# Performance work log

Measured on AMD Instinct MI355X. Metric: run time of the kernel, lower is better.

## Reference

```python
import jax, jax.numpy as jnp
import numpy as np

B, S, D = 2, 2048, 1024
H = 16
HD = D // H  # 64


def setup_inputs() -> dict:
    key = jax.random.key(0)
    ks = jax.random.split(key, 6)
    scale = 0.02
    return {
        "x": jax.random.normal(ks[0], (B, S, D), dtype=jnp.float32),
        "Wq": jax.random.normal(ks[1], (D, D), dtype=jnp.float32) * scale,
        "Wk": jax.random.normal(ks[2], (D, D), dtype=jnp.float32) * scale,
        "Wv": jax.random.normal(ks[3], (D, D), dtype=jnp.float32) * scale,
        "Wo": jax.random.normal(ks[4], (D, D), dtype=jnp.float32) * scale,
        "bo": jnp.zeros((D,), dtype=jnp.float32),
    }


def reference(x, Wq, Wk, Wv, Wo, bo):
    b, n, _ = x.shape
    # QKV projections (weights stored as [d_in, d_out]; no qkv bias)
    q = (x @ Wq).reshape(b, n, H, HD).transpose(0, 2, 1, 3)  # [b,h,n,hd]
    k = (x @ Wk).reshape(b, n, H, HD).transpose(0, 2, 1, 3)
    v = (x @ Wv).reshape(b, n, H, HD).transpose(0, 2, 1, 3)
    # raw scores, causal mask (upper-triangular -> -inf), THEN scale (as in source)
    scores = jnp.einsum("bhqd,bhkd->bhqk", q, k)
    causal = jnp.triu(jnp.ones((n, n), dtype=bool), k=1)
    scores = jnp.where(causal, -jnp.inf, scores)
    attn = jax.nn.softmax(scores / np.sqrt(HD).astype(np.float32), axis=-1)
    # dropout p=0.0 -> identity
    ctx = jnp.einsum("bhqk,bhkd->bqhd", attn, v).reshape(b, n, H * HD)
    return ctx @ Wo + bo
```

## Files before the change

kernel.cpp:

```cpp
#include <hip/hip_runtime.h>
#include <math.h>

#define BB 2
#define SS 2048
#define DD 1024
#define HH 16
#define HDIM 64
#define NTOK (BB * SS)

typedef __attribute__((ext_vector_type(8))) short short8;
typedef __attribute__((ext_vector_type(4))) short short4v;
typedef __attribute__((ext_vector_type(4))) float f32x4;

__device__ __forceinline__ short f2bf(float f) {
    unsigned u = __builtin_bit_cast(unsigned, f);
    u = (u + 0x7FFFu + ((u >> 16) & 1u)) >> 16;
    return (short)u;
}

__device__ __forceinline__ void gl_lds16(const short* g, short* l) {
    __builtin_amdgcn_global_load_lds(
        (const __attribute__((address_space(1))) void*)g,
        (__attribute__((address_space(3))) void*)l, 16, 0, 0);
}

__global__ __launch_bounds__(256) void convert_x_kernel(
    const float* __restrict__ x, short* __restrict__ xbf)
{
    const size_t idx = ((size_t)blockIdx.x * 256 + threadIdx.x) * 8;
    float4 a = *reinterpret_cast<const float4*>(x + idx);
    float4 b = *reinterpret_cast<const float4*>(x + idx + 4);
    short8 o;
    o[0] = f2bf(a.x); o[1] = f2bf(a.y); o[2] = f2bf(a.z); o[3] = f2bf(a.w);
    o[4] = f2bf(b.x); o[5] = f2bf(b.y); o[6] = f2bf(b.z); o[7] = f2bf(b.w);
    *reinterpret_cast<short8*>(xbf + idx) = o;
}

__global__ __launch_bounds__(256) void convw_kernel(
    const float* __restrict__ Wq, const float* __restrict__ Wk,
    const float* __restrict__ Wv, const float* __restrict__ Wo,
    short* __restrict__ Wtq, short* __restrict__ Wtk,
    short* __restrict__ Wtv, short* __restrict__ Wto)
{
    const int z = blockIdx.z;
    const float* W = (z == 0) ? Wq : (z == 1) ? Wk : (z == 2) ? Wv : Wo;
    short* Wt = (z == 0) ? Wtq : (z == 1) ? Wtk : (z == 2) ? Wtv : Wto;
    const int k0 = blockIdx.x * 64, n0 = blockIdx.y * 64;
    __shared__ float T[64][65];
    const int tid = threadIdx.x;
    for (int i = tid; i < 1024; i += 256) {
        int r = i >> 4, c4 = (i & 15) * 4;
        float4 v = *reinterpret_cast<const float4*>(W + (size_t)(k0 + r) * DD + n0 + c4);
        T[r][c4 + 0] = v.x; T[r][c4 + 1] = v.y; T[r][c4 + 2] = v.z; T[r][c4 + 3] = v.w;
    }
    __syncthreads();
    for (int i = tid; i < 512; i += 256) {
        int n = i >> 3, k8 = (i & 7) * 8;
        short8 o;
        #pragma unroll
        for (int j = 0; j < 8; ++j) o[j] = f2bf(T[k8 + j][n]);
        *reinterpret_cast<short8*>(Wt + (size_t)(n0 + n) * DD + k0 + k8) = o;
    }
}

__global__ __launch_bounds__(256) void qkv_mfma_kernel(
    const short* __restrict__ xbf,
    const short* __restrict__ Wtq, const short* __restrict__ Wtk,
    const short* __restrict__ Wtv,
    short* __restrict__ Q, short* __restrict__ K, short* __restrict__ Vt)
{
    const int which = blockIdx.z;
    const short* Wt = (which == 0) ? Wtq : (which == 1) ? Wtk : Wtv;

    const int row0 = blockIdx.y * 128;
    const int col0 = blockIdx.x * 128;
    __shared__ short As[128 * 32];
    __shared__ short Bs[128 * 32];

    const int tid = threadIdx.x;
    const int w = tid >> 6, lane = tid & 63;
    const int wm = (w >> 1) * 64, wn = (w & 1) * 64;
    const int lrow = lane & 15, lgrp = lane >> 4, lk = lgrp * 8;

    f32x4 acc[4][4];
    #pragma unroll
    for (int m = 0; m < 4; ++m)
        #pragma unroll
        for (int n = 0; n < 4; ++n) acc[m][n] = (f32x4){0.f, 0.f, 0.f, 0.f};

    for (int k0 = 0; k0 < DD; k0 += 32) {
        #pragma unroll
        for (int c = 0; c < 2; ++c) {
            int slot = c * 256 + tid;
            int r = slot >> 2, cb = (slot & 3) * 8;
            gl_lds16(xbf + (size_t)(row0 + r) * DD + k0 + cb, As + slot * 8);
            gl_lds16(Wt + (size_t)(col0 + r) * DD + k0 + cb, Bs + slot * 8);
        }
        __syncthreads();
        short8 af[4], bf_[4];
        #pragma unroll
        for (int m = 0; m < 4; ++m)
            af[m] = *reinterpret_cast<const short8*>(&As[(wm + m * 16 + lrow) * 32 + lk]);
        #pragma unroll
        for (int n = 0; n < 4; ++n)
            bf_[n] = *reinterpret_cast<const short8*>(&Bs[(wn + n * 16 + lrow) * 32 + lk]);
        #pragma unroll
        for (int m = 0; m < 4; ++m)
            #pragma unroll
            for (int n = 0; n < 4; ++n)
                acc[m][n] = __builtin_amdgcn_mfma_f32_16x16x32_bf16(
                    af[m], bf_[n], acc[m][n], 0, 0, 0);
        __syncthreads();
    }

    if (which < 2) {
        short* Out = (which == 0) ? Q : K;
        #pragma unroll
        for (int m = 0; m < 4; ++m) {
            #pragma unroll
            for (int r = 0; r < 4; ++r) {
                int tok = row0 + wm + m * 16 + lgrp * 4 + r;
                int bb = tok >> 11, s = tok & 2047;
                #pragma unroll
                for (int n = 0; n < 4; ++n) {
                    int d = col0 + wn + n * 16 + lrow;
                    int hh = d >> 6, hd = d & 63;
                    Out[(((size_t)bb * HH + hh) * SS + s) * HDIM + hd] = f2bf(acc[m][n][r]);
                }
            }
        }
    } else {
        #pragma unroll
        for (int m = 0; m < 4; ++m) {
            int tok0 = row0 + wm + m * 16 + lgrp * 4;
            int bb = tok0 >> 11, s0 = tok0 & 2047;
            #pragma unroll
            for (int n = 0; n < 4; ++n) {
                int d = col0 + wn + n * 16 + lrow;
                int hh = d >> 6, hd = d & 63;
                short4v pk;
                pk[0] = f2bf(acc[m][n][0]); pk[1] = f2bf(acc[m][n][1]);
                pk[2] = f2bf(acc[m][n][2]); pk[3] = f2bf(acc[m][n][3]);
                *reinterpret_cast<short4v*>(
                    Vt + (((size_t)bb * HH + hh) * HDIM + hd) * SS + s0) = pk;
            }
        }
    }
}

__global__ __launch_bounds__(256) void attn_mfma_kernel(
    const short* __restrict__ Q, const short* __restrict__ K,
    const short* __restrict__ Vt, short* __restrict__ ctx)
{
    const int qt = 63 - (int)blockIdx.x;
    const int h = blockIdx.y, b = blockIdx.z;
    const int q0 = qt * 32;

    __shared__ float merge_buf[4][32][68];
    __shared__ float mbuf[4][32], lbuf[4][32];

    const int tid = threadIdx.x;
    const int w = tid >> 6, lane = tid & 63;
    const int lrow = lane & 15, lgrp = lane >> 4;
    short (*Ps)[72] = reinterpret_cast<short (*)[72]>(&merge_buf[w][0][0]);

    const size_t hb = ((size_t)b * HH + h) * SS;
    const float SC = 0.125f * 1.44269504088896340736f;

    short8 qf[2][2];
    const short* Qb = Q + (hb + q0) * HDIM;
    #pragma unroll
    for (int mf = 0; mf < 2; ++mf)
        #pragma unroll
        for (int kf = 0; kf < 2; ++kf)
            qf[mf][kf] = *reinterpret_cast<const short8*>(
                Qb + (mf * 16 + lrow) * HDIM + kf * 32 + lgrp * 8);

    f32x4 Oa[2][4];
    float mrun[2], lrun[2];
    #pragma unroll
    for (int mf = 0; mf < 2; ++mf) {
        #pragma unroll
        for (int nf = 0; nf < 4; ++nf) Oa[mf][nf] = (f32x4){0.f, 0.f, 0.f, 0.f};
        mrun[mf] = -INFINITY; lrun[mf] = 0.f;
    }

    const int nkb = (qt >> 1) + 1;
    const short* Kbase = K + hb * HDIM;
    const short* Vtb = Vt + ((size_t)b * HH + h) * HDIM * SS;

    for (int kb = w; kb < nkb; kb += 4) {
        const int kv0 = kb * 64;

        short8 kfr[4][2];
        #pragma unroll
        for (int nf = 0; nf < 4; ++nf)
            #pragma unroll
            for (int kf = 0; kf < 2; ++kf)
                kfr[nf][kf] = *reinterpret_cast<const short8*>(
                    Kbase + (size_t)(kv0 + nf * 16 + lrow) * HDIM + kf * 32 + lgrp * 8);

        f32x4 s[4][2];
        #pragma unroll
        for (int nf = 0; nf < 4; ++nf)
            #pragma unroll
            for (int mf = 0; mf < 2; ++mf) s[nf][mf] = (f32x4){0.f, 0.f, 0.f, 0.f};
        #pragma unroll
        for (int nf = 0; nf < 4; ++nf)
            #pragma unroll
            for (int mf = 0; mf < 2; ++mf)
                #pragma unroll
                for (int kf = 0; kf < 2; ++kf)
                    s[nf][mf] = __builtin_amdgcn_mfma_f32_16x16x32_bf16(
                        kfr[nf][kf], qf[mf][kf], s[nf][mf], 0, 0, 0);

        const bool diag = (kv0 + 63 > q0);
        #pragma unroll
        for (int nf = 0; nf < 4; ++nf)
            #pragma unroll
            for (int mf = 0; mf < 2; ++mf)
                #pragma unroll
                for (int r = 0; r < 4; ++r) {
                    float v = s[nf][mf][r] * SC;
                    if (diag) {
                        int qg = q0 + mf * 16 + lrow;
                        int kg = kv0 + nf * 16 + lgrp * 4 + r;
                        if (kg > qg) v = -INFINITY;
                    }
                    s[nf][mf][r] = v;
                }

        float alpha[2];
        #pragma unroll
        for (int mf = 0; mf < 2; ++mf) {
            float pm = -INFINITY;
            #pragma unroll
            for (int nf = 0; nf < 4; ++nf)
                #pragma unroll
                for (int r = 0; r < 4; ++r) pm = fmaxf(pm, s[nf][mf][r]);
            pm = fmaxf(pm, __shfl_xor(pm, 16));
            pm = fmaxf(pm, __shfl_xor(pm, 32));
            float mn = fmaxf(mrun[mf], pm);
            alpha[mf] = exp2f(mrun[mf] - mn);
            mrun[mf] = mn;
            float rs = 0.f;
            #pragma unroll
            for (int nf = 0; nf < 4; ++nf)
                #pragma unroll
                for (int r = 0; r < 4; ++r) {
                    float p = exp2f(s[nf][mf][r] - mn);
                    s[nf][mf][r] = p;
                    rs += p;
                }
            rs += __shfl_xor(rs, 16);
            rs += __shfl_xor(rs, 32);
            lrun[mf] = lrun[mf] * alpha[mf] + rs;
        }

        #pragma unroll
        for (int mf = 0; mf < 2; ++mf)
            #pragma unroll
            for (int nf = 0; nf < 4; ++nf) {
                short4v pk;
                pk[0] = f2bf(s[nf][mf][0]); pk[1] = f2bf(s[nf][mf][1]);
                pk[2] = f2bf(s[nf][mf][2]); pk[3] = f2bf(s[nf][mf][3]);
                *reinterpret_cast<short4v*>(&Ps[mf * 16 + lrow][nf * 16 + lgrp * 4]) = pk;
            }
        asm volatile("s_waitcnt lgkmcnt(0)" ::: "memory");
        __builtin_amdgcn_sched_barrier(0);

        short8 pa[2][2], vb_[4][2];
        #pragma unroll
        for (int mf = 0; mf < 2; ++mf)
            #pragma unroll
            for (int kf = 0; kf < 2; ++kf)
                pa[mf][kf] = *reinterpret_cast<const short8*>(
                    &Ps[mf * 16 + lrow][kf * 32 + lgrp * 8]);

        #pragma unroll
        for (int nf = 0; nf < 4; ++nf)
            #pragma unroll
            for (int kf = 0; kf < 2; ++kf)
                vb_[nf][kf] = *reinterpret_cast<const short8*>(
                    Vtb + (size_t)(nf * 16 + lrow) * SS + kv0 + kf * 32 + lgrp * 8);

        #pragma unroll
        for (int mf = 0; mf < 2; ++mf)
            #pragma unroll
            for (int r = 0; r < 4; ++r) {
                float a = __shfl(alpha[mf], lgrp * 4 + r);
                #pragma unroll
                for (int nf = 0; nf < 4; ++nf) Oa[mf][nf][r] *= a;
            }

        #pragma unroll
        for (int mf = 0; mf < 2; ++mf)
            #pragma unroll
            for (int nf = 0; nf < 4; ++nf)
                #pragma unroll
                for (int kf = 0; kf < 2; ++kf)
                    Oa[mf][nf] = __builtin_amdgcn_mfma_f32_16x16x32_bf16(
                        pa[mf][kf], vb_[nf][kf], Oa[mf][nf], 0, 0, 0);
    }

    #pragma unroll
    for (int mf = 0; mf < 2; ++mf) {
        if (lgrp == 0) {
            mbuf[w][mf * 16 + lrow] = mrun[mf];
            lbuf[w][mf * 16 + lrow] = lrun[mf];
        }
        #pragma unroll
        for (int r = 0; r < 4; ++r) {
            int row = mf * 16 + lgrp * 4 + r;
            #pragma unroll
            for (int nf = 0; nf < 4; ++nf)
                merge_buf[w][row][nf * 16 + lrow] = Oa[mf][nf][r];
        }
    }
    __syncthreads();

    {
        const int row = tid >> 3;
        const int c0 = (tid & 7) * 8;
        float m0 = mbuf[0][row], m1 = mbuf[1][row];
        float m2 = mbuf[2][row], m3 = mbuf[3][row];
        float mg = fmaxf(fmaxf(m0, m1), fmaxf(m2, m3));
        float w0 = exp2f(m0 - mg), w1 = exp2f(m1 - mg);
        float w2 = exp2f(m2 - mg), w3 = exp2f(m3 - mg);
        float lg = w0 * lbuf[0][row] + w1 * lbuf[1][row] +
                   w2 * lbuf[2][row] + w3 * lbuf[3][row];
        float rl = 1.f / lg;
        short8 o8;
        #pragma unroll
        for (int j = 0; j < 8; ++j) {
            float o = w0 * merge_buf[0][row][c0 + j] + w1 * merge_buf[1][row][c0 + j] +
                      w2 * merge_buf[2][row][c0 + j] + w3 * merge_buf[3][row][c0 + j];
            o8[j] = f2bf(o * rl);
        }
        const int tok = b * SS + q0 + row;
        *reinterpret_cast<short8*>(ctx + (size_t)tok * DD + h * HDIM + c0) = o8;
    }
}

__global__ __launch_bounds__(256) void out_mfma_kernel(
    const short* __restrict__ ctxbf, const short* __restrict__ Wto,
    const float* __restrict__ bo, float* __restrict__ out)
{
    const int row0 = blockIdx.y * 128;
    const int col0 = blockIdx.x * 128;
    __shared__ short As[128 * 32];
    __shared__ short Bs[128 * 32];

    const int tid = threadIdx.x;
    const int w = tid >> 6, lane = tid & 63;
    const int wm = (w >> 1) * 64, wn = (w & 1) * 64;
    const int lrow = lane & 15, lgrp = lane >> 4, lk = lgrp * 8;

    f32x4 acc[4][4];
    #pragma unroll
    for (int m = 0; m < 4; ++m)
        #pragma unroll
        for (int n = 0; n < 4; ++n) acc[m][n] = (f32x4){0.f, 0.f, 0.f, 0.f};

    for (int k0 = 0; k0 < DD; k0 += 32) {
        #pragma unroll
        for (int c = 0; c < 2; ++c) {
            int slot = c * 256 + tid;
            int r = slot >> 2, cb = (slot & 3) * 8;
            gl_lds16(ctxbf + (size_t)(row0 + r) * DD + k0 + cb, As + slot * 8);
            gl_lds16(Wto + (size_t)(col0 + r) * DD + k0 + cb, Bs + slot * 8);
        }
        __syncthreads();
        short8 af[4], bf_[4];
        #pragma unroll
        for (int m = 0; m < 4; ++m)
            af[m] = *reinterpret_cast<const short8*>(&As[(wm + m * 16 + lrow) * 32 + lk]);
        #pragma unroll
        for (int n = 0; n < 4; ++n)
            bf_[n] = *reinterpret_cast<const short8*>(&Bs[(wn + n * 16 + lrow) * 32 + lk]);
        #pragma unroll
        for (int m = 0; m < 4; ++m)
            #pragma unroll
            for (int n = 0; n < 4; ++n)
                acc[m][n] = __builtin_amdgcn_mfma_f32_16x16x32_bf16(
                    af[m], bf_[n], acc[m][n], 0, 0, 0);
        __syncthreads();
    }

    #pragma unroll
    for (int m = 0; m < 4; ++m) {
        #pragma unroll
        for (int r = 0; r < 4; ++r) {
            int tok = row0 + wm + m * 16 + lgrp * 4 + r;
            #pragma unroll
            for (int n = 0; n < 4; ++n) {
                int d = col0 + wn + n * 16 + lrow;
                out[(size_t)tok * DD + d] = acc[m][n][r] + bo[d];
            }
        }
    }
}

extern "C" void kernel_launch(void* const* d_in, const int* in_sizes, int n_in,
                              void* d_out, int out_size, void* d_ws, size_t ws_size,
                              hipStream_t stream) {
    const float* x  = (const float*)d_in[0];
    const float* Wq = (const float*)d_in[1];
    const float* Wk = (const float*)d_in[2];
    const float* Wv = (const float*)d_in[3];
    const float* Wo = (const float*)d_in[4];
    const float* bo = (const float*)d_in[5];
    float* out = (float*)d_out;

    const size_t plane = (size_t)NTOK * DD;
    const size_t wsz   = (size_t)DD * DD;
    short* xbf  = (short*)d_ws;
    short* Wtq  = xbf + plane;
    short* Wtk  = Wtq + wsz;
    short* Wtv  = Wtk + wsz;
    short* Wto  = Wtv + wsz;
    short* Qb   = Wto + wsz;
    short* Kb   = Qb + plane;
    short* Vtb  = Kb + plane;
    short* ctxb = Vtb + plane;

    convert_x_kernel<<<dim3((unsigned)(plane / (256 * 8))), 256, 0, stream>>>(x, xbf);
    convw_kernel<<<dim3(16, 16, 4), 256, 0, stream>>>(Wq, Wk, Wv, Wo, Wtq, Wtk, Wtv, Wto);
    qkv_mfma_kernel<<<dim3(DD / 128, NTOK / 128, 3), 256, 0, stream>>>(
        xbf, Wtq, Wtk, Wtv, Qb, Kb, Vtb);
    attn_mfma_kernel<<<dim3(SS / 32, HH, BB), 256, 0, stream>>>(Qb, Kb, Vtb, ctxb);
    out_mfma_kernel<<<dim3(DD / 128, NTOK / 128), 256, 0, stream>>>(ctxb, Wto, bo, out);
}
```

Measured before the change: 270.8 us.

## Shrink GEMM tiles, swizzle attention block order, transpose PV MFMA operands

```diff
diff --git a/kernel.cpp b/kernel.cpp
--- a/kernel.cpp
+++ b/kernel.cpp
@@ -73,20 +73,20 @@
     const short* Wt = (which == 0) ? Wtq : (which == 1) ? Wtk : Wtv;
 
     const int row0 = blockIdx.y * 128;
-    const int col0 = blockIdx.x * 128;
+    const int col0 = blockIdx.x * 64;
     __shared__ short As[128 * 32];
-    __shared__ short Bs[128 * 32];
+    __shared__ short Bs[64 * 32];
 
     const int tid = threadIdx.x;
     const int w = tid >> 6, lane = tid & 63;
-    const int wm = (w >> 1) * 64, wn = (w & 1) * 64;
+    const int wm = (w >> 1) * 64, wn = (w & 1) * 32;
     const int lrow = lane & 15, lgrp = lane >> 4, lk = lgrp * 8;
 
-    f32x4 acc[4][4];
+    f32x4 acc[4][2];
     #pragma unroll
     for (int m = 0; m < 4; ++m)
         #pragma unroll
-        for (int n = 0; n < 4; ++n) acc[m][n] = (f32x4){0.f, 0.f, 0.f, 0.f};
+        for (int n = 0; n < 2; ++n) acc[m][n] = (f32x4){0.f, 0.f, 0.f, 0.f};
 
     for (int k0 = 0; k0 < DD; k0 += 32) {
         #pragma unroll
@@ -94,20 +94,23 @@
             int slot = c * 256 + tid;
             int r = slot >> 2, cb = (slot & 3) * 8;
             gl_lds16(xbf + (size_t)(row0 + r) * DD + k0 + cb, As + slot * 8);
-            gl_lds16(Wt + (size_t)(col0 + r) * DD + k0 + cb, Bs + slot * 8);
+        }
+        {
+            int r = tid >> 2, cb = (tid & 3) * 8;
+            gl_lds16(Wt + (size_t)(col0 + r) * DD + k0 + cb, Bs + tid * 8);
         }
         __syncthreads();
-        short8 af[4], bf_[4];
+        short8 af[4], bf_[2];
         #pragma unroll
         for (int m = 0; m < 4; ++m)
             af[m] = *reinterpret_cast<const short8*>(&As[(wm + m * 16 + lrow) * 32 + lk]);
         #pragma unroll
-        for (int n = 0; n < 4; ++n)
+        for (int n = 0; n < 2; ++n)
             bf_[n] = *reinterpret_cast<const short8*>(&Bs[(wn + n * 16 + lrow) * 32 + lk]);
         #pragma unroll
         for (int m = 0; m < 4; ++m)
             #pragma unroll
-            for (int n = 0; n < 4; ++n)
+            for (int n = 0; n < 2; ++n)
                 acc[m][n] = __builtin_amdgcn_mfma_f32_16x16x32_bf16(
                     af[m], bf_[n], acc[m][n], 0, 0, 0);
         __syncthreads();
@@ -122,7 +125,7 @@
                 int tok = row0 + wm + m * 16 + lgrp * 4 + r;
                 int bb = tok >> 11, s = tok & 2047;
                 #pragma unroll
-                for (int n = 0; n < 4; ++n) {
+                for (int n = 0; n < 2; ++n) {
                     int d = col0 + wn + n * 16 + lrow;
                     int hh = d >> 6, hd = d & 63;
                     Out[(((size_t)bb * HH + hh) * SS + s) * HDIM + hd] = f2bf(acc[m][n][r]);
@@ -135,7 +138,7 @@
             int tok0 = row0 + wm + m * 16 + lgrp * 4;
             int bb = tok0 >> 11, s0 = tok0 & 2047;
             #pragma unroll
-            for (int n = 0; n < 4; ++n) {
+            for (int n = 0; n < 2; ++n) {
                 int d = col0 + wn + n * 16 + lrow;
                 int hh = d >> 6, hd = d & 63;
                 short4v pk;
@@ -152,8 +155,11 @@
     const short* __restrict__ Q, const short* __restrict__ K,
     const short* __restrict__ Vt, short* __restrict__ ctx)
 {
-    const int qt = 63 - (int)blockIdx.x;
-    const int h = blockIdx.y, b = blockIdx.z;
+    const int id = (int)(blockIdx.x + 64u * (blockIdx.y + 16u * blockIdx.z));
+    const int swz = (id & 7) * 256 + (id >> 3);
+    const int qt = 63 - (swz & 63);
+    const int hb = swz >> 6;
+    const int h = hb & 15, b = hb >> 4;
     const int q0 = qt * 32;
 
     __shared__ float merge_buf[4][32][68];
@@ -164,11 +170,11 @@
     const int lrow = lane & 15, lgrp = lane >> 4;
     short (*Ps)[72] = reinterpret_cast<short (*)[72]>(&merge_buf[w][0][0]);
 
-    const size_t hb = ((size_t)b * HH + h) * SS;
+    const size_t hb_off = ((size_t)b * HH + h) * SS;
     const float SC = 0.125f * 1.44269504088896340736f;
 
     short8 qf[2][2];
-    const short* Qb = Q + (hb + q0) * HDIM;
+    const short* Qb = Q + (hb_off + q0) * HDIM;
     #pragma unroll
     for (int mf = 0; mf < 2; ++mf)
         #pragma unroll
@@ -176,17 +182,17 @@
             qf[mf][kf] = *reinterpret_cast<const short8*>(
                 Qb + (mf * 16 + lrow) * HDIM + kf * 32 + lgrp * 8);
 
-    f32x4 Oa[2][4];
+    f32x4 Oa[4][2];
     float mrun[2], lrun[2];
     #pragma unroll
-    for (int mf = 0; mf < 2; ++mf) {
-        #pragma unroll
-        for (int nf = 0; nf < 4; ++nf) Oa[mf][nf] = (f32x4){0.f, 0.f, 0.f, 0.f};
-        mrun[mf] = -INFINITY; lrun[mf] = 0.f;
-    }
+    for (int nf = 0; nf < 4; ++nf)
+        #pragma unroll
+        for (int mf = 0; mf < 2; ++mf) Oa[nf][mf] = (f32x4){0.f, 0.f, 0.f, 0.f};
+    mrun[0] = mrun[1] = -INFINITY;
+    lrun[0] = lrun[1] = 0.f;
 
     const int nkb = (qt >> 1) + 1;
-    const short* Kbase = K + hb * HDIM;
+    const short* Kbase = K + hb_off * HDIM;
     const short* Vtb = Vt + ((size_t)b * HH + h) * HDIM * SS;
 
     for (int kb = w; kb < nkb; kb += 4) {
@@ -285,22 +291,21 @@
                     Vtb + (size_t)(nf * 16 + lrow) * SS + kv0 + kf * 32 + lgrp * 8);
 
         #pragma unroll
-        for (int mf = 0; mf < 2; ++mf)
-            #pragma unroll
-            for (int r = 0; r < 4; ++r) {
-                float a = __shfl(alpha[mf], lgrp * 4 + r);
-                #pragma unroll
-                for (int nf = 0; nf < 4; ++nf) Oa[mf][nf][r] *= a;
-            }
-
-        #pragma unroll
-        for (int mf = 0; mf < 2; ++mf)
-            #pragma unroll
-            for (int nf = 0; nf < 4; ++nf)
+        for (int nf = 0; nf < 4; ++nf)
+            #pragma unroll
+            for (int mf = 0; mf < 2; ++mf)
+                #pragma unroll
+                for (int r = 0; r < 4; ++r)
+                    Oa[nf][mf][r] *= alpha[mf];
+
+        #pragma unroll
+        for (int nf = 0; nf < 4; ++nf)
+            #pragma unroll
+            for (int mf = 0; mf < 2; ++mf)
                 #pragma unroll
                 for (int kf = 0; kf < 2; ++kf)
-                    Oa[mf][nf] = __builtin_amdgcn_mfma_f32_16x16x32_bf16(
-                        pa[mf][kf], vb_[nf][kf], Oa[mf][nf], 0, 0, 0);
+                    Oa[nf][mf] = __builtin_amdgcn_mfma_f32_16x16x32_bf16(
+                        vb_[nf][kf], pa[mf][kf], Oa[nf][mf], 0, 0, 0);
     }
 
     #pragma unroll
@@ -310,12 +315,9 @@
             lbuf[w][mf * 16 + lrow] = lrun[mf];
         }
         #pragma unroll
-        for (int r = 0; r < 4; ++r) {
-            int row = mf * 16 + lgrp * 4 + r;
-            #pragma unroll
-            for (int nf = 0; nf < 4; ++nf)
-                merge_buf[w][row][nf * 16 + lrow] = Oa[mf][nf][r];
-        }
+        for (int nf = 0; nf < 4; ++nf)
+            *reinterpret_cast<f32x4*>(
+                &merge_buf[w][mf * 16 + lrow][nf * 16 + lgrp * 4]) = Oa[nf][mf];
     }
     __syncthreads();
 
@@ -346,54 +348,52 @@
     const short* __restrict__ ctxbf, const short* __restrict__ Wto,
     const float* __restrict__ bo, float* __restrict__ out)
 {
-    const int row0 = blockIdx.y * 128;
-    const int col0 = blockIdx.x * 128;
-    __shared__ short As[128 * 32];
-    __shared__ short Bs[128 * 32];
+    const int row0 = blockIdx.y * 64;
+    const int col0 = blockIdx.x * 64;
+    __shared__ short As[64 * 32];
+    __shared__ short Bs[64 * 32];
 
     const int tid = threadIdx.x;
     const int w = tid >> 6, lane = tid & 63;
-    const int wm = (w >> 1) * 64, wn = (w & 1) * 64;
+    const int wm = (w >> 1) * 32, wn = (w & 1) * 32;
     const int lrow = lane & 15, lgrp = lane >> 4, lk = lgrp * 8;
 
-    f32x4 acc[4][4];
-    #pragma unroll
-    for (int m = 0; m < 4; ++m)
-        #pragma unroll
-        for (int n = 0; n < 4; ++n) acc[m][n] = (f32x4){0.f, 0.f, 0.f, 0.f};
+    f32x4 acc[2][2];
+    #pragma unroll
+    for (int m = 0; m < 2; ++m)
+        #pragma unroll
+        for (int n = 0; n < 2; ++n) acc[m][n] = (f32x4){0.f, 0.f, 0.f, 0.f};
 
     for (int k0 = 0; k0 < DD; k0 += 32) {
-        #pragma unroll
-        for (int c = 0; c < 2; ++c) {
-            int slot = c * 256 + tid;
-            int r = slot >> 2, cb = (slot & 3) * 8;
-            gl_lds16(ctxbf + (size_t)(row0 + r) * DD + k0 + cb, As + slot * 8);
-            gl_lds16(Wto + (size_t)(col0 + r) * DD + k0 + cb, Bs + slot * 8);
+        {
+            int r = tid >> 2, cb = (tid & 3) * 8;
+            gl_lds16(ctxbf + (size_t)(row0 + r) * DD + k0 + cb, As + tid * 8);
+            gl_lds16(Wto + (size_t)(col0 + r) * DD + k0 + cb, Bs + tid * 8);
         }
         __syncthreads();
-        short8 af[4], bf_[4];
-        #pragma unroll
-        for (int m = 0; m < 4; ++m)
+        short8 af[2], bf_[2];
+        #pragma unroll
+        for (int m = 0; m < 2; ++m)
             af[m] = *reinterpret_cast<const short8*>(&As[(wm + m * 16 + lrow) * 32 + lk]);
         #pragma unroll
-        for (int n = 0; n < 4; ++n)
+        for (int n = 0; n < 2; ++n)
             bf_[n] = *reinterpret_cast<const short8*>(&Bs[(wn + n * 16 + lrow) * 32 + lk]);
         #pragma unroll
-        for (int m = 0; m < 4; ++m)
-            #pragma unroll
-            for (int n = 0; n < 4; ++n)
+        for (int m = 0; m < 2; ++m)
+            #pragma unroll
+            for (int n = 0; n < 2; ++n)
                 acc[m][n] = __builtin_amdgcn_mfma_f32_16x16x32_bf16(
                     af[m], bf_[n], acc[m][n], 0, 0, 0);
         __syncthreads();
     }
 
     #pragma unroll
-    for (int m = 0; m < 4; ++m) {
+    for (int m = 0; m < 2; ++m) {
         #pragma unroll
         for (int r = 0; r < 4; ++r) {
             int tok = row0 + wm + m * 16 + lgrp * 4 + r;
             #pragma unroll
-            for (int n = 0; n < 4; ++n) {
+            for (int n = 0; n < 2; ++n) {
                 int d = col0 + wn + n * 16 + lrow;
                 out[(size_t)tok * DD + d] = acc[m][n][r] + bo[d];
             }
@@ -426,8 +426,8 @@
 
     convert_x_kernel<<<dim3((unsigned)(plane / (256 * 8))), 256, 0, stream>>>(x, xbf);
     convw_kernel<<<dim3(16, 16, 4), 256, 0, stream>>>(Wq, Wk, Wv, Wo, Wtq, Wtk, Wtv, Wto);
-    qkv_mfma_kernel<<<dim3(DD / 128, NTOK / 128, 3), 256, 0, stream>>>(
+    qkv_mfma_kernel<<<dim3(DD / 64, NTOK / 128, 3), 256, 0, stream>>>(
         xbf, Wtq, Wtk, Wtv, Qb, Kb, Vtb);
     attn_mfma_kernel<<<dim3(SS / 32, HH, BB), 256, 0, stream>>>(Qb, Kb, Vtb, ctxb);
-    out_mfma_kernel<<<dim3(DD / 128, NTOK / 128), 256, 0, stream>>>(ctxb, Wto, bo, out);
-}
+    out_mfma_kernel<<<dim3(DD / 64, NTOK / 64), 256, 0, stream>>>(ctxb, Wto, bo, out);
+}
```

Result: faster. 224.6 us (-17.1%).
